# Kernel tuning notes

Measured on AMD Instinct MI355X. Metric: run time of the kernel, lower is better.

## Reference

```python
import jax, jax.numpy as jnp
import numpy as np

IGNORE_INDEX = -100


def setup_inputs() -> dict:
    key = jax.random.key(0)
    k1, k2, k3 = jax.random.split(key, 3)
    BT, H, V = 2048, 2048, 128000
    x = jax.random.normal(k1, (BT, H), dtype=jnp.float32)
    weight = jax.random.normal(k2, (V, H), dtype=jnp.float32) * (1.0 / np.sqrt(H))
    target = jax.random.randint(k3, (BT,), 0, V, dtype=jnp.int64)
    return {"x": x, "weight": weight, "target": target}


def reference(x, weight, target):
    # Fused linear + cross-entropy forward (reduction='mean').
    # logits: [BT, V], accumulated in fp32 like the helion kernel.
    logits = jnp.einsum("bh,vh->bv", x.astype(jnp.float32), weight.astype(jnp.float32))
    lse = jax.nn.logsumexp(logits, axis=-1)  # [BT]
    target_logit = jnp.take_along_axis(logits, target[:, None], axis=-1)[:, 0]
    valid = (target != IGNORE_INDEX)
    nll = (lse - target_logit) * valid.astype(jnp.float32)  # [BT]
    n_non_ignore = valid.sum().astype(jnp.float32)
    loss = nll.sum() / n_non_ignore
    return loss.astype(x.dtype), lse
```

## Files before the change

kernel.cpp:

```cpp
#include <hip/hip_runtime.h>
#include <hip/hip_bf16.h>


typedef __bf16 bf16x8 __attribute__((ext_vector_type(8)));
typedef float f32x4  __attribute__((ext_vector_type(4)));
typedef float f32x16 __attribute__((ext_vector_type(16)));

#define BM 128
#define BN 128
#define BK 32
#define LDK 40

__device__ __forceinline__ unsigned pkbf(float a, float b) {
  __hip_bfloat162 h = __float22bfloat162_rn(float2{a, b});
  unsigned r;
  __builtin_memcpy(&r, &h, 4);
  return r;
}

__device__ __forceinline__ void gl16(const void* g, const void* l) {
  using GP = const unsigned __attribute__((address_space(1)))*;
  using LP = unsigned __attribute__((address_space(3)))*;
  __builtin_amdgcn_global_load_lds((GP)(unsigned long long)g,
                                   (LP)(unsigned)(unsigned long long)l, 16, 0, 0);
}

__global__ __launch_bounds__(256)
void k_cvt256(const float* __restrict__ src, __bf16* __restrict__ dst, int H, int NT)
{
  const int bid = blockIdx.x;
  const int kt = bid % NT;
  const int r = threadIdx.x;
  const float* s = src + (size_t)((bid / NT) * 256 + r) * H + kt * 64;
  __bf16* d = dst + (size_t)bid * 16384;
  #pragma unroll
  for (int j = 0; j < 8; ++j) {
    float4 f0 = ((const float4*)s)[2 * j];
    float4 f1 = ((const float4*)s)[2 * j + 1];
    uint4 p;
    p.x = pkbf(f0.x, f0.y); p.y = pkbf(f0.z, f0.w);
    p.z = pkbf(f1.x, f1.y); p.w = pkbf(f1.z, f1.w);
    *(uint4*)(d + (j >> 2) * 8192 + (j & 3) * 2048 + r * 8) = p;
  }
}

__global__ __launch_bounds__(256)
void k_tgt(const float* __restrict__ x, const float* __restrict__ w,
           const int* __restrict__ tgt, float* __restrict__ ws_t, int H)
{
  const int row  = blockIdx.x * 4 + (threadIdx.x >> 6);
  const int lane = threadIdx.x & 63;
  const int tv = tgt[row];
  if (tv == -100) { if (lane == 0) ws_t[row] = 0.f; return; }
  const float* xr = x + (size_t)row * H;
  const float* wr = w + (size_t)tv * H;
  float acc = 0.f;
  for (int j = lane * 4; j < H; j += 256) {
    float4 a = *(const float4*)(xr + j);
    float4 b = *(const float4*)(wr + j);
    acc += a.x * b.x + a.y * b.y + a.z * b.z + a.w * b.w;
  }
  #pragma unroll
  for (int m = 1; m < 64; m <<= 1) acc += __shfl_xor(acc, m, 64);
  if (lane == 0) ws_t[row] = acc;
}

#define VM8 asm volatile("s_waitcnt vmcnt(8)" ::: "memory");
#define VM4 asm volatile("s_waitcnt vmcnt(4)" ::: "memory");
#define VM0 asm volatile("s_waitcnt vmcnt(0)" ::: "memory");
#define NOVM

#define SLOT(SL, DO_ST, ST_S, WAITM)                                            \
  {                                                                             \
    const __bf16* Ab = &As[SL][0];                                              \
    const __bf16* Bb = &Bs[SL][0];                                              \
    _Pragma("unroll")                                                           \
    for (int m = 0; m < 4; ++m)                                                 \
      aF[m] = *(const bf16x8*)&Ab[kcoff + (arow + m * 16) * 8];                 \
    _Pragma("unroll")                                                           \
    for (int n = 0; n < 4; ++n)                                                 \
      bF[n] = *(const bf16x8*)&Bb[kcoff + (bcol + n * 16) * 8];                 \
    if (DO_ST) stage_slot(ST_S);                                                \
    __builtin_amdgcn_s_barrier();                                               \
    asm volatile("s_waitcnt lgkmcnt(0)" ::: "memory");                          \
    __builtin_amdgcn_s_setprio(1);                                              \
    _Pragma("unroll")                                                           \
    for (int m = 0; m < 4; ++m)                                                 \
      _Pragma("unroll")                                                         \
      for (int n = 0; n < 4; ++n)                                               \
        acc[m][n] = __builtin_amdgcn_mfma_f32_16x16x32_bf16(aF[m], bF[n],       \
                                                            acc[m][n], 0, 0, 0);\
    __builtin_amdgcn_s_setprio(0);                                              \
    __builtin_amdgcn_s_barrier();                                               \
    _Pragma("unroll")                                                           \
    for (int m = 0; m < 4; ++m)                                                 \
      aF[m] = *(const bf16x8*)&Ab[kcoff + (arow + (m + 4) * 16) * 8];           \
    __builtin_amdgcn_s_barrier();                                               \
    asm volatile("s_waitcnt lgkmcnt(0)" ::: "memory");                          \
    __builtin_amdgcn_s_setprio(1);                                              \
    _Pragma("unroll")                                                           \
    for (int m = 0; m < 4; ++m)                                                 \
      _Pragma("unroll")                                                         \
      for (int n = 0; n < 4; ++n)                                               \
        acc[m + 4][n] = __builtin_amdgcn_mfma_f32_16x16x32_bf16(aF[m], bF[n],   \
                                                         acc[m + 4][n], 0, 0, 0);\
    __builtin_amdgcn_s_setprio(0);                                              \
    WAITM                                                                       \
    __builtin_amdgcn_s_barrier();                                               \
  }

__global__ __launch_bounds__(512, 2)
void k_gemm16(const __bf16* __restrict__ xb, const __bf16* __restrict__ wb,
              float* __restrict__ ws_m, float* __restrict__ ws_s,
              int NT, int NCB, int ROWB)
{
  __shared__ __bf16 As[4][8192];
  __shared__ __bf16 Bs[4][8192];

  int wg = blockIdx.x;
  const int nwg = gridDim.x;
  if ((nwg & 7) == 0) wg = (wg & 7) * (nwg >> 3) + (wg >> 3);
  const int rowb = wg % ROWB;
  const int cb   = wg / ROWB;
  const int row0 = rowb * 256;

  const int t    = threadIdx.x;
  const int lane = t & 63;
  const int wv   = t >> 6;
  const int wr   = wv >> 2;
  const int wc   = wv & 3;

  const int kcoff = (lane >> 4) * 2048;
  const int arow  = wr * 128 + (lane & 15);
  const int bcol  = wc * 64 + (lane & 15);

  const __bf16* ga = xb + (size_t)(rowb * NT) * 16384;
  const __bf16* gb = wb + (size_t)(cb * NT) * 16384;

  auto stage_slot = [&](int s) {
    const int ph = s & 3;
    const size_t off = (size_t)(s >> 1) * 16384 + (size_t)(s & 1) * 8192
                     + wv * 512 + lane * 8;
    const __bf16* a = ga + off;
    const __bf16* b = gb + off;
    gl16(a,        &As[ph][wv * 512]);
    gl16(a + 4096, &As[ph][4096 + wv * 512]);
    gl16(b,        &Bs[ph][wv * 512]);
    gl16(b + 4096, &Bs[ph][4096 + wv * 512]);
  };

  const int S = NT * 2;

  stage_slot(0); stage_slot(1); stage_slot(2);
  VM8
  __builtin_amdgcn_s_barrier();

  f32x4 acc[8][4] = {};
  bf16x8 aF[4], bF[4];

  for (int g = 0; g < (S - 4) / 4; ++g) {
    const int j0 = g * 4;
    SLOT(0, true, j0 + 3, VM8)
    SLOT(1, true, j0 + 4, VM8)
    SLOT(2, true, j0 + 5, VM8)
    SLOT(3, true, j0 + 6, VM8)
  }
  SLOT(0, true,  S - 1, VM8)
  SLOT(1, false, 0,     VM4)
  SLOT(2, false, 0,     VM0)
  SLOT(3, false, 0,     NOVM)

  __syncthreads();

  float* redM = (float*)&As[0][0];
  float* redS = redM + 1024;
  const int g4 = (lane >> 4) * 4;
  #pragma unroll
  for (int m = 0; m < 8; ++m) {
    #pragma unroll
    for (int r = 0; r < 4; ++r) {
      const int rl = wr * 128 + m * 16 + g4 + r;
      float mx = fmaxf(fmaxf(acc[m][0][r], acc[m][1][r]),
                       fmaxf(acc[m][2][r], acc[m][3][r]));
      #pragma unroll
      for (int sh = 1; sh < 16; sh <<= 1) mx = fmaxf(mx, __shfl_xor(mx, sh, 64));
      float sv = 0.f;
      #pragma unroll
      for (int n = 0; n < 4; ++n) sv += expf(acc[m][n][r] - mx);
      #pragma unroll
      for (int sh = 1; sh < 16; sh <<= 1) sv += __shfl_xor(sv, sh, 64);
      if ((lane & 15) == 0) { redM[wc * 256 + rl] = mx; redS[wc * 256 + rl] = sv; }
    }
  }
  __syncthreads();
  if (t < 256) {
    const float m0 = redM[t], m1 = redM[256 + t], m2 = redM[512 + t], m3 = redM[768 + t];
    float M = fmaxf(fmaxf(m0, m1), fmaxf(m2, m3));
    float S2 = redS[t] * expf(m0 - M) + redS[256 + t] * expf(m1 - M)
             + redS[512 + t] * expf(m2 - M) + redS[768 + t] * expf(m3 - M);
    const int grow = row0 + t;
    ws_m[(size_t)grow * NCB + cb] = M;
    ws_s[(size_t)grow * NCB + cb] = S2;
  }
}

__global__ __launch_bounds__(256, 2)
void k_gemm_lse(const float* __restrict__ x, const float* __restrict__ w,
                const int* __restrict__ tgt,
                float* __restrict__ ws_m, float* __restrict__ ws_s,
                float* __restrict__ ws_t,
                int H, int NCB, int ROWB)
{
  __shared__ unsigned short As[2][BM * LDK];
  __shared__ unsigned short Bs[2][BN * LDK];

  const int bid  = blockIdx.x;
  const int rowb = bid % ROWB;
  const int cb   = bid / ROWB;
  const int row0 = rowb * BM;
  const int col0 = cb * BN;

  const int t    = threadIdx.x;
  const int lane = t & 63;
  const int wv   = t >> 6;
  const int sr = t >> 1;
  const int sk = (t & 1) * 16;

  const float* xa = x + (size_t)(row0 + sr) * H + sk;
  const float* wb = w + (size_t)(col0 + sr) * H + sk;

  float4 ra[4], rb[4];
  #pragma unroll
  for (int i = 0; i < 4; ++i) {
    ra[i] = *(const float4*)(xa + i * 4);
    rb[i] = *(const float4*)(wb + i * 4);
  }

  auto stage = [&](int buf) {
    uint4 p0, p1;
    p0.x = pkbf(ra[0].x, ra[0].y); p0.y = pkbf(ra[0].z, ra[0].w);
    p0.z = pkbf(ra[1].x, ra[1].y); p0.w = pkbf(ra[1].z, ra[1].w);
    p1.x = pkbf(ra[2].x, ra[2].y); p1.y = pkbf(ra[2].z, ra[2].w);
    p1.z = pkbf(ra[3].x, ra[3].y); p1.w = pkbf(ra[3].z, ra[3].w);
    *(uint4*)&As[buf][sr * LDK + sk]     = p0;
    *(uint4*)&As[buf][sr * LDK + sk + 8] = p1;
    p0.x = pkbf(rb[0].x, rb[0].y); p0.y = pkbf(rb[0].z, rb[0].w);
    p0.z = pkbf(rb[1].x, rb[1].y); p0.w = pkbf(rb[1].z, rb[1].w);
    p1.x = pkbf(rb[2].x, rb[2].y); p1.y = pkbf(rb[2].z, rb[2].w);
    p1.z = pkbf(rb[3].x, rb[3].y); p1.w = pkbf(rb[3].z, rb[3].w);
    *(uint4*)&Bs[buf][sr * LDK + sk]     = p0;
    *(uint4*)&Bs[buf][sr * LDK + sk + 8] = p1;
  };

  stage(0);
  __syncthreads();

  f32x16 acc[4] = {};
  const int rlo = lane & 31;
  const int hi  = lane >> 5;
  const int NT  = H / BK;
  int cur = 0;

  for (int kt = 0; kt < NT; ++kt) {
    const bool pf = (kt + 1 < NT);
    if (pf) {
      xa += BK; wb += BK;
      #pragma unroll
      for (int i = 0; i < 4; ++i) {
        ra[i] = *(const float4*)(xa + i * 4);
        rb[i] = *(const float4*)(wb + i * 4);
      }
    }
    const unsigned short* A = As[cur];
    const unsigned short* B = Bs[cur];
    #pragma unroll
    for (int ks = 0; ks < 2; ++ks) {
      const int koff = ks * 16 + hi * 8;
      bf16x8 a = *(const bf16x8*)&A[(wv * 32 + rlo) * LDK + koff];
      #pragma unroll
      for (int nf = 0; nf < 4; ++nf) {
        bf16x8 b = *(const bf16x8*)&B[(nf * 32 + rlo) * LDK + koff];
        acc[nf] = __builtin_amdgcn_mfma_f32_32x32x16_bf16(a, b, acc[nf], 0, 0, 0);
      }
    }
    if (pf) stage(cur ^ 1);
    __syncthreads();
    cur ^= 1;
  }

  #pragma unroll
  for (int reg = 0; reg < 16; ++reg) {
    const int row = wv * 32 + (reg & 3) + 8 * (reg >> 2) + 4 * hi;
    float mx = fmaxf(fmaxf(acc[0][reg], acc[1][reg]), fmaxf(acc[2][reg], acc[3][reg]));
    #pragma unroll
    for (int m = 1; m < 32; m <<= 1) mx = fmaxf(mx, __shfl_xor(mx, m, 64));
    float s = 0.f;
    #pragma unroll
    for (int nf = 0; nf < 4; ++nf) s += expf(acc[nf][reg] - mx);
    #pragma unroll
    for (int m = 1; m < 32; m <<= 1) s += __shfl_xor(s, m, 64);
    const int grow = row0 + row;
    if (rlo == 0) {
      ws_m[(size_t)grow * NCB + cb] = mx;
      ws_s[(size_t)grow * NCB + cb] = s;
    }
    const int tv = tgt[grow];
    #pragma unroll
    for (int nf = 0; nf < 4; ++nf) {
      if (tv == col0 + nf * 32 + rlo) ws_t[grow] = acc[nf][reg];
    }
  }
}

__global__ void k_rowlse(const float* __restrict__ ws_m, const float* __restrict__ ws_s,
                         const float* __restrict__ ws_t, const int* __restrict__ tgt,
                         float* __restrict__ out, float* __restrict__ ws_nll, int NCB)
{
  const int row = blockIdx.x;
  const int t = threadIdx.x;
  const float* pm = ws_m + (size_t)row * NCB;
  const float* ps = ws_s + (size_t)row * NCB;
  __shared__ float red[8];

  float M = -3.0e38f;
  for (int j = t; j < NCB; j += 256) M = fmaxf(M, pm[j]);
  #pragma unroll
  for (int m = 1; m < 64; m <<= 1) M = fmaxf(M, __shfl_xor(M, m, 64));
  if ((t & 63) == 0) red[t >> 6] = M;
  __syncthreads();
  M = fmaxf(fmaxf(red[0], red[1]), fmaxf(red[2], red[3]));

  float S = 0.f;
  for (int j = t; j < NCB; j += 256) S += ps[j] * expf(pm[j] - M);
  #pragma unroll
  for (int m = 1; m < 64; m <<= 1) S += __shfl_xor(S, m, 64);
  if ((t & 63) == 0) red[4 + (t >> 6)] = S;
  __syncthreads();

  if (t == 0) {
    S = red[4] + red[5] + red[6] + red[7];
    const float lse = M + logf(S);
    out[1 + row] = lse;
    const int tv = tgt[row];
    ws_nll[row] = (tv != -100) ? (lse - ws_t[row]) : 0.f;
  }
}

__global__ void k_loss(const float* __restrict__ ws_nll, const int* __restrict__ tgt,
                       float* __restrict__ out, int BT)
{
  const int t = threadIdx.x;
  float s = 0.f, c = 0.f;
  for (int i = t; i < BT; i += 256) {
    s += ws_nll[i];
    c += (tgt[i] != -100) ? 1.f : 0.f;
  }
  __shared__ float rs[4], rc[4];
  #pragma unroll
  for (int m = 1; m < 64; m <<= 1) { s += __shfl_xor(s, m, 64); c += __shfl_xor(c, m, 64); }
  if ((t & 63) == 0) { rs[t >> 6] = s; rc[t >> 6] = c; }
  __syncthreads();
  if (t == 0) {
    s = rs[0] + rs[1] + rs[2] + rs[3];
    c = rc[0] + rc[1] + rc[2] + rc[3];
    out[0] = s / c;
  }
}

extern "C" void kernel_launch(void* const* d_in, const int* in_sizes, int n_in,
                              void* d_out, int out_size, void* d_ws, size_t ws_size,
                              hipStream_t stream)
{
  const float* x  = (const float*)d_in[0];
  const float* w  = (const float*)d_in[1];
  const int* tgt  = (const int*)d_in[2];
  float* out      = (float*)d_out;

  const int BT = in_sizes[2];
  const int H  = in_sizes[0] / BT;
  const int V  = in_sizes[1] / H;

  const int NT    = H / 64;
  const int ROWB  = BT / 256;
  const int NCB   = V / 256;

  const size_t bf_elems   = (size_t)BT * H + (size_t)V * H;
  const size_t need_bytes = bf_elems * 2 + ((size_t)2 * BT * NCB + 2 * (size_t)BT) * 4;

  if (ws_size >= need_bytes && (BT % 256) == 0 && (V % 256) == 0 && (H % 128) == 0) {
    __bf16* x_bf = (__bf16*)d_ws;
    __bf16* w_bf = x_bf + (size_t)BT * H;
    float* ws_m   = (float*)(w_bf + (size_t)V * H);
    float* ws_s   = ws_m + (size_t)BT * NCB;
    float* ws_t   = ws_s + (size_t)BT * NCB;
    float* ws_nll = ws_t + BT;

    k_cvt256<<<(V / 256) * NT, 256, 0, stream>>>(w, w_bf, H, NT);
    k_cvt256<<<(BT / 256) * NT, 256, 0, stream>>>(x, x_bf, H, NT);
    k_tgt<<<BT / 4, 256, 0, stream>>>(x, w, tgt, ws_t, H);
    k_gemm16<<<ROWB * NCB, 512, 0, stream>>>(x_bf, w_bf, ws_m, ws_s, NT, NCB, ROWB);
    k_rowlse<<<BT, 256, 0, stream>>>(ws_m, ws_s, ws_t, tgt, out, ws_nll, NCB);
    k_loss<<<1, 256, 0, stream>>>(ws_nll, tgt, out, BT);
  } else {
    const int ROWB1 = BT / BM;
    const int NCB1  = V / BN;
    float* ws_m   = (float*)d_ws;
    float* ws_s   = ws_m + (size_t)BT * NCB1;
    float* ws_t   = ws_s + (size_t)BT * NCB1;
    float* ws_nll = ws_t + BT;

    k_gemm_lse<<<ROWB1 * NCB1, 256, 0, stream>>>(x, w, tgt, ws_m, ws_s, ws_t, H, NCB1, ROWB1);
    k_rowlse<<<BT, 256, 0, stream>>>(ws_m, ws_s, ws_t, tgt, out, ws_nll, NCB1);
    k_loss<<<1, 256, 0, stream>>>(ws_nll, tgt, out, BT);
  }
}
```

Baseline: 1.377 ms.

## Double-buffer LDS fragment registers to prefetch next slot during MFMA

Restructures the GEMM main loop so the A/B fragments for the next K-slot are read from LDS while the second half of the current slot's MFMAs run. B fragments alternate between b0 and b1, and the A halves use a0 and a1. The explicit lgkmcnt waits are dropped and there is one fewer barrier per slot. The goal is to hide LDS read latency behind matrix compute, at the cost of more VGPRs, which could hurt occupancy at 2 waves/SIMD, and a more delicate ordering of barriers against the async LDS stages.

```diff
diff --git a/kernel.cpp b/kernel.cpp
--- a/kernel.cpp
+++ b/kernel.cpp
@@ -69,44 +69,43 @@
 #define VM4 asm volatile("s_waitcnt vmcnt(4)" ::: "memory");
 #define VM0 asm volatile("s_waitcnt vmcnt(0)" ::: "memory");
 #define NOVM
-
-#define SLOT(SL, DO_ST, ST_S, WAITM)                                            \
+#define MEMFENCE asm volatile("" ::: "memory");
+
+#define SLOT(SL, SLN, BCUR, BNXT, DO_ST, ST_S, DO_RA, VMW)                      \
   {                                                                             \
-    const __bf16* Ab = &As[SL][0];                                              \
-    const __bf16* Bb = &Bs[SL][0];                                              \
+    __builtin_amdgcn_s_barrier();                                               \
+    MEMFENCE                                                                    \
+    if (DO_ST) stage_slot(ST_S);                                                \
     _Pragma("unroll")                                                           \
     for (int m = 0; m < 4; ++m)                                                 \
-      aF[m] = *(const bf16x8*)&Ab[kcoff + (arow + m * 16) * 8];                 \
-    _Pragma("unroll")                                                           \
-    for (int n = 0; n < 4; ++n)                                                 \
-      bF[n] = *(const bf16x8*)&Bb[kcoff + (bcol + n * 16) * 8];                 \
-    if (DO_ST) stage_slot(ST_S);                                                \
-    __builtin_amdgcn_s_barrier();                                               \
-    asm volatile("s_waitcnt lgkmcnt(0)" ::: "memory");                          \
+      a1[m] = *(const bf16x8*)&As[SL][kcoff + (arow + (m + 4) * 16) * 8];       \
     __builtin_amdgcn_s_setprio(1);                                              \
     _Pragma("unroll")                                                           \
     for (int m = 0; m < 4; ++m)                                                 \
       _Pragma("unroll")                                                         \
       for (int n = 0; n < 4; ++n)                                               \
-        acc[m][n] = __builtin_amdgcn_mfma_f32_16x16x32_bf16(aF[m], bF[n],       \
+        acc[m][n] = __builtin_amdgcn_mfma_f32_16x16x32_bf16(a0[m], BCUR[n],     \
                                                             acc[m][n], 0, 0, 0);\
     __builtin_amdgcn_s_setprio(0);                                              \
+    VMW                                                                         \
     __builtin_amdgcn_s_barrier();                                               \
-    _Pragma("unroll")                                                           \
-    for (int m = 0; m < 4; ++m)                                                 \
-      aF[m] = *(const bf16x8*)&Ab[kcoff + (arow + (m + 4) * 16) * 8];           \
-    __builtin_amdgcn_s_barrier();                                               \
-    asm volatile("s_waitcnt lgkmcnt(0)" ::: "memory");                          \
+    MEMFENCE                                                                    \
+    if (DO_RA) {                                                                \
+      _Pragma("unroll")                                                         \
+      for (int m = 0; m < 4; ++m)                                               \
+        a0[m] = *(const bf16x8*)&As[SLN][kcoff + (arow + m * 16) * 8];          \
+      _Pragma("unroll")                                                         \
+      for (int n = 0; n < 4; ++n)                                               \
+        BNXT[n] = *(const bf16x8*)&Bs[SLN][kcoff + (bcol + n * 16) * 8];        \
+    }                                                                           \
     __builtin_amdgcn_s_setprio(1);                                              \
     _Pragma("unroll")                                                           \
     for (int m = 0; m < 4; ++m)                                                 \
       _Pragma("unroll")                                                         \
       for (int n = 0; n < 4; ++n)                                               \
-        acc[m + 4][n] = __builtin_amdgcn_mfma_f32_16x16x32_bf16(aF[m], bF[n],   \
+        acc[m + 4][n] = __builtin_amdgcn_mfma_f32_16x16x32_bf16(a1[m], BCUR[n], \
                                                          acc[m + 4][n], 0, 0, 0);\
     __builtin_amdgcn_s_setprio(0);                                              \
-    WAITM                                                                       \
-    __builtin_amdgcn_s_barrier();                                               \
   }
 
 __global__ __launch_bounds__(512, 2)
@@ -154,21 +153,28 @@
   stage_slot(0); stage_slot(1); stage_slot(2);
   VM8
   __builtin_amdgcn_s_barrier();
+  MEMFENCE
 
   f32x4 acc[8][4] = {};
-  bf16x8 aF[4], bF[4];
+  bf16x8 a0[4], a1[4], b0[4], b1[4];
+  #pragma unroll
+  for (int m = 0; m < 4; ++m)
+    a0[m] = *(const bf16x8*)&As[0][kcoff + (arow + m * 16) * 8];
+  #pragma unroll
+  for (int n = 0; n < 4; ++n)
+    b0[n] = *(const bf16x8*)&Bs[0][kcoff + (bcol + n * 16) * 8];
 
   for (int g = 0; g < (S - 4) / 4; ++g) {
     const int j0 = g * 4;
-    SLOT(0, true, j0 + 3, VM8)
-    SLOT(1, true, j0 + 4, VM8)
-    SLOT(2, true, j0 + 5, VM8)
-    SLOT(3, true, j0 + 6, VM8)
-  }
-  SLOT(0, true,  S - 1, VM8)
-  SLOT(1, false, 0,     VM4)
-  SLOT(2, false, 0,     VM0)
-  SLOT(3, false, 0,     NOVM)
+    SLOT(0, 1, b0, b1, true, j0 + 3, true, VM8)
+    SLOT(1, 2, b1, b0, true, j0 + 4, true, VM8)
+    SLOT(2, 3, b0, b1, true, j0 + 5, true, VM8)
+    SLOT(3, 0, b1, b0, true, j0 + 6, true, VM8)
+  }
+  SLOT(0, 1, b0, b1, true,  S - 1, true,  VM8)
+  SLOT(1, 2, b1, b0, false, 0,     true,  VM4)
+  SLOT(2, 3, b0, b1, false, 0,     true,  VM0)
+  SLOT(3, 0, b1, b0, false, 0,     false, NOVM)
 
   __syncthreads();
 
```

Measured after the change: 1.315 ms. -4.5%, faster.
